# Kernel tuning notes

Measured on AMD Instinct MI355X. Metric: run time of the kernel, lower is better.

## Reference

```python
import jax, jax.numpy as jnp
import numpy as np

B, N, D = 4, 2048, 1024
H = 16
HD = D // H  # head_dim = 64
SCALE = HD ** -0.5


def setup_inputs() -> dict:
    key = jax.random.key(0)
    k1, k2, k3, k4 = jax.random.split(key, 4)
    x = jax.random.normal(k1, (B, N, D), dtype=jnp.float32)
    # init-scale weights for numerically sane softmax logits
    w_qkv = jax.random.normal(k2, (3 * D, D), dtype=jnp.float32) * 0.02
    w_proj = jax.random.normal(k3, (D, D), dtype=jnp.float32) * 0.02
    b_proj = jax.random.normal(k4, (D,), dtype=jnp.float32) * 0.02
    return {"x": x, "w_qkv": w_qkv, "w_proj": w_proj, "b_proj": b_proj}


def reference(x, w_qkv, w_proj, b_proj):
    # qkv projection (width_mult=1.0 -> Dyna slicing is identity; qkv_bias=False)
    qkv = jnp.einsum('bnd,ed->bne', x, w_qkv)          # (B, N, 3D)
    qkv = qkv.reshape(B, N, 3, H, HD)
    q = qkv[:, :, 0].transpose(0, 2, 1, 3)              # (B, H, N, HD)
    k = qkv[:, :, 1].transpose(0, 2, 1, 3)
    v = qkv[:, :, 2].transpose(0, 2, 1, 3)
    q = q * SCALE
    attn = jnp.einsum('bhqd,bhkd->bhqk', q, k)          # (B, H, N, N)
    attn = jax.nn.softmax(attn, axis=-1)
    out = jnp.einsum('bhqk,bhkd->bhqd', attn, v)        # (B, H, N, HD)
    out = out.transpose(0, 2, 1, 3).reshape(B, N, D)
    # output projection (bias=True)
    return jnp.einsum('bnd,ed->bne', out, w_proj) + b_proj
```

## Files before the change

kernel.cpp:

```cpp
#include <hip/hip_runtime.h>
#include <hip/hip_bf16.h>
#include <stdint.h>


typedef __attribute__((ext_vector_type(8))) short short8;
typedef __attribute__((ext_vector_type(4))) short short4v;
typedef __attribute__((ext_vector_type(4))) float float4v;
typedef __attribute__((ext_vector_type(16))) float float16v;

#define MFMA16(a, b, c) __builtin_amdgcn_mfma_f32_16x16x32_bf16((a), (b), (c), 0, 0, 0)
#define MFMA32(a, b, c) __builtin_amdgcn_mfma_f32_32x32x16_bf16((a), (b), (c), 0, 0, 0)

static __device__ __forceinline__ unsigned short f2bf(float f) {
  union { float f; unsigned u; } v; v.f = f;
  unsigned r = v.u + 0x7fffu + ((v.u >> 16) & 1u);
  return (unsigned short)(r >> 16);
}
static __device__ __forceinline__ float bf2f(unsigned short u) {
  union { unsigned u; float f; } v; v.u = ((unsigned)u) << 16;
  return v.f;
}
static __device__ __forceinline__ unsigned pkbf(float a, float b) {
  union { __hip_bfloat162 v; unsigned u; } c;
  c.v = __float22bfloat162_rn(make_float2(a, b));
  return c.u;
}
static __device__ __forceinline__ float ex2(float x) {
#if __has_builtin(__builtin_amdgcn_exp2f)
  return __builtin_amdgcn_exp2f(x);
#else
  return exp2f(x);
#endif
}
static __device__ __forceinline__ float4v fzero() {
  float4v z; z[0] = 0.f; z[1] = 0.f; z[2] = 0.f; z[3] = 0.f; return z;
}
static __device__ __forceinline__ float16v fzero16() {
  float16v z;
#pragma unroll
  for (int i = 0; i < 16; ++i) z[i] = 0.f;
  return z;
}
static __device__ __forceinline__ void pl32swap(unsigned& a, unsigned& b) {
  asm volatile("v_permlane32_swap_b32 %0, %1" : "+v"(a), "+v"(b));
}
static __device__ __forceinline__ void load_lds16(const void* g, void* l) {
  typedef const __attribute__((address_space(1))) void* gp_t;
  typedef __attribute__((address_space(3))) void* lp_t;
  __builtin_amdgcn_global_load_lds((gp_t)(uintptr_t)g, (lp_t)(uint32_t)(uintptr_t)l, 16, 0, 0);
}

__global__ void detect_dtype(const unsigned short* __restrict__ x, int* flag) {
  __shared__ int cnt;
  if (threadIdx.x == 0) cnt = 0;
  __syncthreads();
  int c = 0;
  for (int i = threadIdx.x; i < 4096; i += 256) {
    const unsigned v = x[i] & 0x7FFFu;
    if ((v >> 7) >= 134u) ++c;
  }
  atomicAdd(&cnt, c);
  __syncthreads();
  if (threadIdx.x == 0) *flag = (cnt > 64) ? 1 : 0;
}

static __device__ __forceinline__ void cv8(const void* src, unsigned short* dst,
                                           int i, int fl) {
  if (fl) {
    const float4v a = *(const float4v*)((const float*)src + i);
    const float4v b = *(const float4v*)((const float*)src + i + 4);
    short8 o;
    o[0] = (short)f2bf(a[0]); o[1] = (short)f2bf(a[1]);
    o[2] = (short)f2bf(a[2]); o[3] = (short)f2bf(a[3]);
    o[4] = (short)f2bf(b[0]); o[5] = (short)f2bf(b[1]);
    o[6] = (short)f2bf(b[2]); o[7] = (short)f2bf(b[3]);
    *(short8*)(dst + i) = o;
  } else {
    *(short8*)(dst + i) = *(const short8*)((const unsigned short*)src + i);
  }
}
__global__ __launch_bounds__(256) void convert_all(
    const void* __restrict__ s0, const void* __restrict__ s1,
    const void* __restrict__ s2, const void* __restrict__ s3,
    unsigned short* __restrict__ d0, unsigned short* __restrict__ d1,
    unsigned short* __restrict__ d2, unsigned short* __restrict__ d3,
    const int* __restrict__ flag) {
  const int t = blockIdx.x * 256 + threadIdx.x;
  const int fl = *flag;
  if (t < 1048576)       cv8(s0, d0, t * 8, fl);
  else if (t < 1441792)  cv8(s1, d1, (t - 1048576) * 8, fl);
  else if (t < 1572864)  cv8(s2, d2, (t - 1441792) * 8, fl);
  else if (t < 1572992)  cv8(s3, d3, (t - 1572864) * 8, fl);
}

__global__ __launch_bounds__(256) void qkv_gemm(
    const unsigned short* __restrict__ X, const unsigned short* __restrict__ W,
    unsigned short* __restrict__ Qo, unsigned short* __restrict__ Ko,
    unsigned short* __restrict__ Vt) {
  __shared__ __attribute__((aligned(16))) unsigned short lA[4][128 * 32];
  __shared__ __attribute__((aligned(16))) unsigned short lB[4][128 * 32];
  const int tid = threadIdx.x;
  const int wave = tid >> 6, lane = tid & 63, quad = lane >> 4, l16 = lane & 15;
  const int wm = wave >> 1, wn = wave & 1;
  const int m0 = blockIdx.x * 128, n0 = blockIdx.y * 128;

  float4v acc[4][4];
  for (int i = 0; i < 4; ++i) for (int j = 0; j < 4; ++j) acc[i][j] = fzero();

  const int f0 = tid, f1 = 256 + tid;
  const int r0 = f0 >> 2, c0 = (f0 & 3) * 8;
  const int r1 = f1 >> 2, c1 = (f1 & 3) * 8;
  const int dof0 = (wave * 64) * 8;
  const int dof1 = (256 + wave * 64) * 8;

#define QKV_STAGE(buf, k0)                                                   \
  load_lds16(X + (size_t)(m0 + r0) * 1024 + (k0) + c0, lA[buf] + dof0);      \
  load_lds16(X + (size_t)(m0 + r1) * 1024 + (k0) + c1, lA[buf] + dof1);      \
  load_lds16(W + (size_t)(n0 + r0) * 1024 + (k0) + c0, lB[buf] + dof0);      \
  load_lds16(W + (size_t)(n0 + r1) * 1024 + (k0) + c1, lB[buf] + dof1);

#define QKV_COMPUTE(kk)                                                      \
  {                                                                          \
    const unsigned short* sA = lA[(kk) & 3];                                 \
    const unsigned short* sB = lB[(kk) & 3];                                 \
    short8 af[4], bfr[4];                                                    \
    for (int t = 0; t < 4; ++t) {                                            \
      af[t]  = *(const short8*)(sA + (wm * 64 + t * 16 + l16) * 32 + quad * 8); \
      bfr[t] = *(const short8*)(sB + (wn * 64 + t * 16 + l16) * 32 + quad * 8); \
    }                                                                        \
    for (int mt = 0; mt < 4; ++mt)                                           \
      for (int nt = 0; nt < 4; ++nt)                                         \
        acc[mt][nt] = MFMA16(af[mt], bfr[nt], acc[mt][nt]);                  \
  }

  QKV_STAGE(0, 0);
  QKV_STAGE(1, 32);
  for (int k = 0; k < 30; ++k) {
    QKV_STAGE((k + 2) & 3, k * 32 + 64);
    asm volatile("s_waitcnt vmcnt(8)" ::: "memory");
    __builtin_amdgcn_s_barrier();
    QKV_COMPUTE(k);
  }
  asm volatile("s_waitcnt vmcnt(4)" ::: "memory");
  __builtin_amdgcn_s_barrier();
  QKV_COMPUTE(30);
  asm volatile("s_waitcnt vmcnt(0)" ::: "memory");
  __builtin_amdgcn_s_barrier();
  QKV_COMPUTE(31);
#undef QKV_STAGE
#undef QKV_COMPUTE

  const float QSCALE = 0.18033688011112042f;
  for (int mt = 0; mt < 4; ++mt) {
    const int mbase = m0 + wm * 64 + mt * 16 + quad * 4;
    const int b = mbase >> 11;
    const int nrow = mbase & 2047;
    for (int nt = 0; nt < 4; ++nt) {
      const int e = n0 + wn * 64 + nt * 16 + l16;
      const int c = e >> 10, h = (e >> 6) & 15, hd = e & 63;
      const int bh = b * 16 + h;
      if (c == 0) {
        for (int r = 0; r < 4; ++r)
          Qo[((size_t)bh * 2048 + nrow + r) * 64 + hd] = f2bf(acc[mt][nt][r] * QSCALE);
      } else if (c == 1) {
        for (int r = 0; r < 4; ++r)
          Ko[((size_t)bh * 2048 + nrow + r) * 64 + hd] = f2bf(acc[mt][nt][r]);
      } else {
        short4v pk;
        for (int r = 0; r < 4; ++r) pk[r] = (short)f2bf(acc[mt][nt][r]);
        *(short4v*)(Vt + ((size_t)bh * 64 + hd) * 2048 + nrow) = pk;
      }
    }
  }
}

__global__ __launch_bounds__(256, 4) void flash_attn(
    const unsigned short* __restrict__ Q, const unsigned short* __restrict__ K,
    const unsigned short* __restrict__ Vt, unsigned short* __restrict__ AO) {
  __shared__ __attribute__((aligned(16))) unsigned short lK[2][64 * 72];
  __shared__ __attribute__((aligned(16))) unsigned short lV[2][64 * 72];
  const int tid = threadIdx.x;
  const int wave = tid >> 6, lane = tid & 63;
  const int l31 = lane & 31, hi = lane >> 5;
  const int qt = blockIdx.x, bh = blockIdx.y;
  const int b = bh >> 4, h = bh & 15;
  const size_t base = (size_t)bh * 2048 * 64;
  const unsigned short* Qp = Q + base;
  const unsigned short* Kp = K + base;
  const unsigned short* Vp = Vt + base;
  const int q0 = qt * 128;

  const int qa = q0 + wave * 32 + l31;
  short8 qf[4];
#pragma unroll
  for (int j = 0; j < 4; ++j)
    qf[j] = *(const short8*)(Qp + (size_t)qa * 64 + j * 16 + hi * 8);

  float16v oacc0 = fzero16(), oacc1 = fzero16();
  float lsum = 0.f;

  const int f0 = tid, f1 = 256 + tid;
  const int sk0 = (f0 >> 3) * 72 + (f0 & 7) * 8;
  const int sk1 = (f1 >> 3) * 72 + (f1 & 7) * 8;

  short8 kv0 = *(const short8*)(Kp + f0 * 8);
  short8 kv1 = *(const short8*)(Kp + f1 * 8);
  short8 vv0 = *(const short8*)(Vp + (size_t)(f0 >> 3) * 2048 + (f0 & 7) * 8);
  short8 vv1 = *(const short8*)(Vp + (size_t)(f1 >> 3) * 2048 + (f1 & 7) * 8);

  for (int kb = 0; kb < 32; ++kb) {
    unsigned short* const Kb = lK[kb & 1];
    unsigned short* const Vb = lV[kb & 1];
    *(short8*)(Kb + sk0) = kv0;
    *(short8*)(Kb + sk1) = kv1;
    *(short8*)(Vb + sk0) = vv0;
    *(short8*)(Vb + sk1) = vv1;
    __syncthreads();
    if (kb < 31) {
      const size_t ko = (size_t)(kb + 1) * 4096;
      kv0 = *(const short8*)(Kp + ko + f0 * 8);
      kv1 = *(const short8*)(Kp + ko + f1 * 8);
      vv0 = *(const short8*)(Vp + (size_t)(f0 >> 3) * 2048 + (kb + 1) * 64 + (f0 & 7) * 8);
      vv1 = *(const short8*)(Vp + (size_t)(f1 >> 3) * 2048 + (kb + 1) * 64 + (f1 & 7) * 8);
    }

#pragma unroll
    for (int kb2 = 0; kb2 < 2; ++kb2) {
      const unsigned short* krow = Kb + (kb2 * 32 + l31) * 72 + hi * 8;
      float16v s = fzero16();
#pragma unroll
      for (int j = 0; j < 4; ++j)
        s = MFMA32(*(const short8*)(krow + j * 16), qf[j], s);

      unsigned u[8];
      float ls = 0.f;
#pragma unroll
      for (int j = 0; j < 8; ++j) {
        const float e0 = ex2(s[2 * j]);
        const float e1 = ex2(s[2 * j + 1]);
        ls += e0 + e1;
        u[j] = pkbf(e0, e1);
      }
      lsum += ls;

      pl32swap(u[0], u[2]); pl32swap(u[1], u[3]);
      pl32swap(u[4], u[6]); pl32swap(u[5], u[7]);
      union { unsigned w[4]; short8 s8; } fr0, fr1;
      fr0.w[0] = u[0]; fr0.w[1] = u[1]; fr0.w[2] = u[2]; fr0.w[3] = u[3];
      fr1.w[0] = u[4]; fr1.w[1] = u[5]; fr1.w[2] = u[6]; fr1.w[3] = u[7];

      const unsigned short* vrow0 = Vb + l31 * 72 + kb2 * 32 + hi * 8;
      const unsigned short* vrow1 = vrow0 + 32 * 72;
      oacc0 = MFMA32(*(const short8*)(vrow0), fr0.s8, oacc0);
      oacc1 = MFMA32(*(const short8*)(vrow1), fr0.s8, oacc1);
      oacc0 = MFMA32(*(const short8*)(vrow0 + 16), fr1.s8, oacc0);
      oacc1 = MFMA32(*(const short8*)(vrow1 + 16), fr1.s8, oacc1);
    }
  }

  lsum += __shfl_xor(lsum, 32);
  const float inv = 1.f / lsum;

  unsigned short* ao = AO + ((size_t)(b * 2048 + qa)) * 1024 + h * 64 + hi * 4;
#pragma unroll
  for (int mt = 0; mt < 2; ++mt) {
    const float16v& oc = mt ? oacc1 : oacc0;
#pragma unroll
    for (int g = 0; g < 4; ++g) {
      union { unsigned u2[2]; short4v s4; } o;
      o.u2[0] = pkbf(oc[4 * g] * inv, oc[4 * g + 1] * inv);
      o.u2[1] = pkbf(oc[4 * g + 2] * inv, oc[4 * g + 3] * inv);
      *(short4v*)(ao + mt * 32 + g * 8) = o.s4;
    }
  }
}

__global__ __launch_bounds__(256) void proj_gemm(
    const unsigned short* __restrict__ A, const unsigned short* __restrict__ W,
    const unsigned short* __restrict__ bias_bf, const void* __restrict__ bias_raw,
    void* __restrict__ outv, const int* __restrict__ flag) {
  __shared__ __attribute__((aligned(16))) unsigned short lA[4][128 * 32];
  __shared__ __attribute__((aligned(16))) unsigned short lB[4][128 * 32];
  const int tid = threadIdx.x;
  const int wave = tid >> 6, lane = tid & 63, quad = lane >> 4, l16 = lane & 15;
  const int wm = wave >> 1, wn = wave & 1;
  const int m0 = blockIdx.x * 128, n0 = blockIdx.y * 128;
  const int fl = *flag;

  float4v acc[4][4];
  for (int i = 0; i < 4; ++i) for (int j = 0; j < 4; ++j) acc[i][j] = fzero();

  const int f0 = tid, f1 = 256 + tid;
  const int r0 = f0 >> 2, c0 = (f0 & 3) * 8;
  const int r1 = f1 >> 2, c1 = (f1 & 3) * 8;
  const int dof0 = (wave * 64) * 8;
  const int dof1 = (256 + wave * 64) * 8;

#define PROJ_STAGE(buf, k0)                                                  \
  load_lds16(A + (size_t)(m0 + r0) * 1024 + (k0) + c0, lA[buf] + dof0);      \
  load_lds16(A + (size_t)(m0 + r1) * 1024 + (k0) + c1, lA[buf] + dof1);      \
  load_lds16(W + (size_t)(n0 + r0) * 1024 + (k0) + c0, lB[buf] + dof0);      \
  load_lds16(W + (size_t)(n0 + r1) * 1024 + (k0) + c1, lB[buf] + dof1);

#define PROJ_COMPUTE(kk)                                                     \
  {                                                                          \
    const unsigned short* sA = lA[(kk) & 3];                                 \
    const unsigned short* sB = lB[(kk) & 3];                                 \
    short8 af[4], bfr[4];                                                    \
    for (int t = 0; t < 4; ++t) {                                            \
      af[t]  = *(const short8*)(sA + (wm * 64 + t * 16 + l16) * 32 + quad * 8); \
      bfr[t] = *(const short8*)(sB + (wn * 64 + t * 16 + l16) * 32 + quad * 8); \
    }                                                                        \
    for (int mt = 0; mt < 4; ++mt)                                           \
      for (int nt = 0; nt < 4; ++nt)                                         \
        acc[mt][nt] = MFMA16(af[mt], bfr[nt], acc[mt][nt]);                  \
  }

  PROJ_STAGE(0, 0);
  PROJ_STAGE(1, 32);
  for (int k = 0; k < 30; ++k) {
    PROJ_STAGE((k + 2) & 3, k * 32 + 64);
    asm volatile("s_waitcnt vmcnt(8)" ::: "memory");
    __builtin_amdgcn_s_barrier();
    PROJ_COMPUTE(k);
  }
  asm volatile("s_waitcnt vmcnt(4)" ::: "memory");
  __builtin_amdgcn_s_barrier();
  PROJ_COMPUTE(30);
  asm volatile("s_waitcnt vmcnt(0)" ::: "memory");
  __builtin_amdgcn_s_barrier();
  PROJ_COMPUTE(31);
#undef PROJ_STAGE
#undef PROJ_COMPUTE

  for (int mt = 0; mt < 4; ++mt) {
    const int mbase = m0 + wm * 64 + mt * 16 + quad * 4;
    for (int nt = 0; nt < 4; ++nt) {
      const int e = n0 + wn * 64 + nt * 16 + l16;
      const float bv = fl ? ((const float*)bias_raw)[e] : bf2f(bias_bf[e]);
      for (int r = 0; r < 4; ++r) {
        const float val = acc[mt][nt][r] + bv;
        const size_t idx = (size_t)(mbase + r) * 1024 + e;
        if (fl) ((float*)outv)[idx] = val;
        else    ((unsigned short*)outv)[idx] = f2bf(val);
      }
    }
  }
}

extern "C" void kernel_launch(void* const* d_in, const int* in_sizes, int n_in,
                              void* d_out, int out_size, void* d_ws, size_t ws_size,
                              hipStream_t stream) {
  const void* x_raw     = d_in[0];
  const void* wqkv_raw  = d_in[1];
  const void* wproj_raw = d_in[2];
  const void* bproj_raw = d_in[3];

  const size_t NE = (size_t)4 * 16 * 2048 * 64;
  unsigned short* ws = (unsigned short*)d_ws;
  unsigned short* Q      = ws;
  unsigned short* K      = Q + NE;
  unsigned short* Vt     = K + NE;
  unsigned short* xb     = Vt + NE;
  unsigned short* AO     = xb;
  unsigned short* wqkvb  = xb + NE;
  unsigned short* wprojb = wqkvb + 3145728;
  unsigned short* bprojb = wprojb + 1048576;
  int* flag = (int*)(bprojb + 1024);

  detect_dtype<<<1, 256, 0, stream>>>((const unsigned short*)x_raw, flag);
  convert_all<<<6145, 256, 0, stream>>>(x_raw, wqkv_raw, wproj_raw, bproj_raw,
                                        xb, wqkvb, wprojb, bprojb, flag);

  qkv_gemm<<<dim3(64, 24), 256, 0, stream>>>(xb, wqkvb, Q, K, Vt);
  flash_attn<<<dim3(16, 64), 256, 0, stream>>>(Q, K, Vt, AO);
  proj_gemm<<<dim3(64, 8), 256, 0, stream>>>(AO, wprojb, bprojb, bproj_raw,
                                             d_out, flag);
}
```

Before: 282.0 us.

## Restructure QKV GEMM into 256x256 tiles with swizzled LDS and interleaved staging

The QKV projection GEMM moves from 128x128 tiles with 256 threads to 256x256 tiles with 512 threads (8 waves, each producing 128x64). The K dimension is staged in 64-wide chunks into a double-buffered, XOR-swizzled LDS layout. Global-to-LDS loads for the next chunk are interleaved with MFMA phases, with s_setprio raising priority during the math. The goal is more operand reuse per LDS byte, fewer bank conflicts, and better overlap of loads with compute. In exchange there are far fewer blocks (384 vs 1536), which risks poor CU occupancy and tail effects, plus higher register and LDS use per block.

```diff
diff --git a/kernel.cpp b/kernel.cpp
--- a/kernel.cpp
+++ b/kernel.cpp
@@ -93,81 +93,118 @@
   else if (t < 1572992)  cv8(s3, d3, (t - 1572864) * 8, fl);
 }
 
-__global__ __launch_bounds__(256) void qkv_gemm(
+__global__ __launch_bounds__(512) void qkv_gemm(
     const unsigned short* __restrict__ X, const unsigned short* __restrict__ W,
     unsigned short* __restrict__ Qo, unsigned short* __restrict__ Ko,
     unsigned short* __restrict__ Vt) {
-  __shared__ __attribute__((aligned(16))) unsigned short lA[4][128 * 32];
-  __shared__ __attribute__((aligned(16))) unsigned short lB[4][128 * 32];
+  __shared__ __attribute__((aligned(16))) unsigned short lA[2][2 * 128 * 64];
+  __shared__ __attribute__((aligned(16))) unsigned short lB[2][2 * 128 * 64];
   const int tid = threadIdx.x;
   const int wave = tid >> 6, lane = tid & 63, quad = lane >> 4, l16 = lane & 15;
-  const int wm = wave >> 1, wn = wave & 1;
-  const int m0 = blockIdx.x * 128, n0 = blockIdx.y * 128;
-
-  float4v acc[4][4];
-  for (int i = 0; i < 4; ++i) for (int j = 0; j < 4; ++j) acc[i][j] = fzero();
-
-  const int f0 = tid, f1 = 256 + tid;
-  const int r0 = f0 >> 2, c0 = (f0 & 3) * 8;
-  const int r1 = f1 >> 2, c1 = (f1 & 3) * 8;
+  const int wr = wave >> 2, wc = wave & 3;
+  const int m0 = blockIdx.x * 256, n0 = blockIdx.y * 256;
+
+  float4v acc[8][4];
+#pragma unroll
+  for (int i = 0; i < 8; ++i)
+#pragma unroll
+    for (int j = 0; j < 4; ++j) acc[i][j] = fzero();
+
+  const int rbase = tid >> 3;
+  const int scol = (tid & 7) ^ (rbase & 7);
   const int dof0 = (wave * 64) * 8;
-  const int dof1 = (256 + wave * 64) * 8;
-
-#define QKV_STAGE(buf, k0)                                                   \
-  load_lds16(X + (size_t)(m0 + r0) * 1024 + (k0) + c0, lA[buf] + dof0);      \
-  load_lds16(X + (size_t)(m0 + r1) * 1024 + (k0) + c1, lA[buf] + dof1);      \
-  load_lds16(W + (size_t)(n0 + r0) * 1024 + (k0) + c0, lB[buf] + dof0);      \
-  load_lds16(W + (size_t)(n0 + r1) * 1024 + (k0) + c1, lB[buf] + dof1);
-
-#define QKV_COMPUTE(kk)                                                      \
-  {                                                                          \
-    const unsigned short* sA = lA[(kk) & 3];                                 \
-    const unsigned short* sB = lB[(kk) & 3];                                 \
-    short8 af[4], bfr[4];                                                    \
-    for (int t = 0; t < 4; ++t) {                                            \
-      af[t]  = *(const short8*)(sA + (wm * 64 + t * 16 + l16) * 32 + quad * 8); \
-      bfr[t] = *(const short8*)(sB + (wn * 64 + t * 16 + l16) * 32 + quad * 8); \
-    }                                                                        \
-    for (int mt = 0; mt < 4; ++mt)                                           \
-      for (int nt = 0; nt < 4; ++nt)                                         \
-        acc[mt][nt] = MFMA16(af[mt], bfr[nt], acc[mt][nt]);                  \
-  }
-
-  QKV_STAGE(0, 0);
-  QKV_STAGE(1, 32);
-  for (int k = 0; k < 30; ++k) {
-    QKV_STAGE((k + 2) & 3, k * 32 + 64);
-    asm volatile("s_waitcnt vmcnt(8)" ::: "memory");
-    __builtin_amdgcn_s_barrier();
-    QKV_COMPUTE(k);
-  }
-  asm volatile("s_waitcnt vmcnt(4)" ::: "memory");
-  __builtin_amdgcn_s_barrier();
-  QKV_COMPUTE(30);
+  const int dof1 = (512 + wave * 64) * 8;
+
+#define QSTAGE(u, sT)                                                         \
+  {                                                                           \
+    const int sb_ = (sT) & 1;                                                 \
+    const int kk_ = ((sT) & 15) * 64;                                         \
+    if ((u) < 2) {                                                            \
+      load_lds16(X + (size_t)(m0 + (u) * 128 + rbase) * 1024 + kk_ + scol * 8,\
+                 lA[sb_] + (u) * 8192 + dof0);                                \
+      load_lds16(X + (size_t)(m0 + (u) * 128 + 64 + rbase) * 1024 + kk_ + scol * 8,\
+                 lA[sb_] + (u) * 8192 + dof1);                                \
+    } else {                                                                  \
+      load_lds16(W + (size_t)(n0 + ((u)-2) * 128 + rbase) * 1024 + kk_ + scol * 8,\
+                 lB[sb_] + ((u)-2) * 8192 + dof0);                            \
+      load_lds16(W + (size_t)(n0 + ((u)-2) * 128 + 64 + rbase) * 1024 + kk_ + scol * 8,\
+                 lB[sb_] + ((u)-2) * 8192 + dof1);                            \
+    }                                                                         \
+  }
+
+  QSTAGE(0, 0); QSTAGE(1, 0); QSTAGE(2, 0); QSTAGE(3, 0);
   asm volatile("s_waitcnt vmcnt(0)" ::: "memory");
   __builtin_amdgcn_s_barrier();
-  QKV_COMPUTE(31);
-#undef QKV_STAGE
-#undef QKV_COMPUTE
+
+  const unsigned short* const Ah0 = lA[0] + wr * 8192;
+  const unsigned short* const Ah1 = lA[1] + wr * 8192;
+  const unsigned short* const Bh0 = lB[0] + (wc >> 1) * 8192;
+  const unsigned short* const Bh1 = lB[1] + (wc >> 1) * 8192;
+  const int rB0 = (wc & 1) * 64;
+  const int lsw = l16 & 7;
+
+  for (int i = 0; i < 8; ++i) {
+#pragma unroll
+    for (int p = 0; p < 8; ++p) {
+      const int cb = p >> 2;
+      const int mg = p & 1, ng = (p >> 1) & 1;
+      const unsigned short* Ah = cb ? Ah1 : Ah0;
+      const unsigned short* Bh = cb ? Bh1 : Bh0;
+      short8 af[4][2], bfv[2][2];
+#pragma unroll
+      for (int m4 = 0; m4 < 4; ++m4) {
+        const int rowA = (mg * 4 + m4) * 16 + l16;
+#pragma unroll
+        for (int ks = 0; ks < 2; ++ks)
+          af[m4][ks] = *(const short8*)(Ah + rowA * 64 + (((ks * 4 + quad) ^ lsw) * 8));
+      }
+#pragma unroll
+      for (int n2 = 0; n2 < 2; ++n2) {
+        const int rowB = rB0 + (ng * 2 + n2) * 16 + l16;
+#pragma unroll
+        for (int ks = 0; ks < 2; ++ks)
+          bfv[n2][ks] = *(const short8*)(Bh + rowB * 64 + (((ks * 4 + quad) ^ lsw) * 8));
+      }
+      QSTAGE(p & 3, 2 * i + 1 + cb);
+      if ((p & 3) == 3) asm volatile("s_waitcnt vmcnt(0)" ::: "memory");
+      __builtin_amdgcn_s_barrier();
+      __builtin_amdgcn_sched_barrier(0);
+      __builtin_amdgcn_s_setprio(1);
+#pragma unroll
+      for (int m4 = 0; m4 < 4; ++m4)
+#pragma unroll
+        for (int n2 = 0; n2 < 2; ++n2)
+#pragma unroll
+          for (int ks = 0; ks < 2; ++ks)
+            acc[mg * 4 + m4][ng * 2 + n2] =
+                MFMA16(af[m4][ks], bfv[n2][ks], acc[mg * 4 + m4][ng * 2 + n2]);
+      __builtin_amdgcn_s_setprio(0);
+      __builtin_amdgcn_s_barrier();
+    }
+  }
+#undef QSTAGE
 
   const float QSCALE = 0.18033688011112042f;
-  for (int mt = 0; mt < 4; ++mt) {
-    const int mbase = m0 + wm * 64 + mt * 16 + quad * 4;
-    const int b = mbase >> 11;
-    const int nrow = mbase & 2047;
-    for (int nt = 0; nt < 4; ++nt) {
-      const int e = n0 + wn * 64 + nt * 16 + l16;
-      const int c = e >> 10, h = (e >> 6) & 15, hd = e & 63;
+  const int cclass = n0 >> 10;
+#pragma unroll
+  for (int mf = 0; mf < 8; ++mf) {
+    const int mrow = m0 + wr * 128 + mf * 16 + quad * 4;
+    const int b = mrow >> 11;
+    const int nrow = mrow & 2047;
+#pragma unroll
+    for (int nf = 0; nf < 4; ++nf) {
+      const int e = n0 + wc * 64 + nf * 16 + l16;
+      const int h = (e >> 6) & 15, hd = e & 63;
       const int bh = b * 16 + h;
-      if (c == 0) {
+      if (cclass == 0) {
         for (int r = 0; r < 4; ++r)
-          Qo[((size_t)bh * 2048 + nrow + r) * 64 + hd] = f2bf(acc[mt][nt][r] * QSCALE);
-      } else if (c == 1) {
+          Qo[((size_t)bh * 2048 + nrow + r) * 64 + hd] = f2bf(acc[mf][nf][r] * QSCALE);
+      } else if (cclass == 1) {
         for (int r = 0; r < 4; ++r)
-          Ko[((size_t)bh * 2048 + nrow + r) * 64 + hd] = f2bf(acc[mt][nt][r]);
+          Ko[((size_t)bh * 2048 + nrow + r) * 64 + hd] = f2bf(acc[mf][nf][r]);
       } else {
         short4v pk;
-        for (int r = 0; r < 4; ++r) pk[r] = (short)f2bf(acc[mt][nt][r]);
+        for (int r = 0; r < 4; ++r) pk[r] = (short)f2bf(acc[mf][nf][r]);
         *(short4v*)(Vt + ((size_t)bh * 64 + hd) * 2048 + nrow) = pk;
       }
     }
@@ -372,7 +409,7 @@
   convert_all<<<6145, 256, 0, stream>>>(x_raw, wqkv_raw, wproj_raw, bproj_raw,
                                         xb, wqkvb, wprojb, bprojb, flag);
 
-  qkv_gemm<<<dim3(64, 24), 256, 0, stream>>>(xb, wqkvb, Q, K, Vt);
+  qkv_gemm<<<dim3(32, 12), 512, 0, stream>>>(xb, wqkvb, Q, K, Vt);
   flash_attn<<<dim3(16, 64), 256, 0, stream>>>(Q, K, Vt, AO);
   proj_gemm<<<dim3(64, 8), 256, 0, stream>>>(AO, wprojb, bprojb, bproj_raw,
                                              d_out, flag);
```

After: 289.4 us. 1.03x slower.
